# Kernel optimization log

Hardware: AMD Instinct MI355X
Metric: run time of the kernel (lower is better)

## Reference

```python
import jax, jax.numpy as jnp
import numpy as np

TT_SHAPES = [16, 16, 16, 16, 16, 16]
TT_RANKS = [1, 64, 64, 64, 64, 64, 1]
OUT_FEATURES = 4096  # 16*16*16
IN_FEATURES = 4096   # 16*16*16
N_TOKENS = 8192


def setup_inputs() -> dict:
    key = jax.random.key(0)
    ks = jax.random.split(key, len(TT_SHAPES) + 2)
    inp = {}
    for i in range(len(TT_SHAPES)):
        shape = (TT_RANKS[i], TT_SHAPES[i], TT_RANKS[i + 1])
        # xavier-uniform-like init
        fan = TT_RANKS[i] * TT_SHAPES[i] + TT_SHAPES[i] * TT_RANKS[i + 1]
        bound = float(np.sqrt(6.0 / fan))
        inp[f"core{i}"] = jax.random.uniform(ks[i], shape, jnp.float32, -bound, bound)
    inp["x"] = jax.random.normal(ks[-2], (N_TOKENS, IN_FEATURES), dtype=jnp.float32)
    b_bound = 1.0 / np.sqrt(IN_FEATURES)
    inp["b"] = jax.random.uniform(ks[-1], (OUT_FEATURES,), jnp.float32, -b_bound, b_bound)
    return inp


def _recover_weight(cores):
    # chain of reshape+matmul contractions, exactly as TTLinearR._recover_weight
    w = cores[0]
    for i in range(1, len(cores)):
        w = w.reshape(-1, TT_RANKS[i]) @ cores[i].reshape(TT_RANKS[i], -1)
    return w.reshape(OUT_FEATURES, IN_FEATURES)


def reference(x, core0, core1, core2, core3, core4, core5, b):
    w = _recover_weight([core0, core1, core2, core3, core4, core5])
    # F.linear(x, w, b) == x @ w.T + b
    return x @ w.T + b
```

## Files before the change

kernel.cpp:

```cpp
#include <hip/hip_runtime.h>


#define TOK 8192
#define DIN 4096
#define DOUT 4096
#define RNK 64

#define TB 16
#define BK 256
#define NKI (DIN / BK)
#define XS 264
#define TSTR 66

#define G2M 128
#define G2N 256
#define AS 72

typedef __bf16 bf16x8 __attribute__((ext_vector_type(8)));
typedef float f32x4 __attribute__((ext_vector_type(4)));
typedef float f32x16 __attribute__((ext_vector_type(16)));

__device__ __forceinline__ unsigned short f2bf(float f) {
  unsigned int u = __float_as_uint(f);
  u += 0x7FFFu + ((u >> 16) & 1u);
  return (unsigned short)(u >> 16);
}

__global__ void chain1(const float* __restrict__ c0, const float* __restrict__ c1,
                       const float* __restrict__ c4, const float* __restrict__ c5,
                       float* __restrict__ S1, float* __restrict__ S3) {
  int b = blockIdx.x;
  if (b < 64) {
    int idx = b * 256 + threadIdx.x;
    int m = idx >> 10, n = idx & 1023;
    const float* a = c0 + m * 64;
    float acc = 0.f;
#pragma unroll
    for (int k = 0; k < 64; ++k) acc += a[k] * c1[k * 1024 + n];
    S1[idx] = acc;
  } else {
    int idx = (b - 64) * 256 + threadIdx.x;
    int m = idx >> 4, n = idx & 15;
    const float* a = c4 + m * 64;
    float acc = 0.f;
#pragma unroll
    for (int k = 0; k < 64; ++k) acc += a[k] * c5[k * 16 + n];
    S3[idx] = acc;
  }
}

__global__ void chain2(const float* __restrict__ S1, const float* __restrict__ c2,
                       const float* __restrict__ c3, const float* __restrict__ S3,
                       unsigned short* __restrict__ Abf, unsigned short* __restrict__ Bbf) {
  int b = blockIdx.x;
  if (b < 1024) {
    int idx = b * 256 + threadIdx.x;
    int m = idx >> 10, n = idx & 1023;
    const float* a = S1 + m * 64;
    float acc = 0.f;
#pragma unroll
    for (int k = 0; k < 64; ++k) acc += a[k] * c2[k * 1024 + n];
    Abf[idx] = f2bf(acc);
  } else {
    int idx = (b - 1024) * 256 + threadIdx.x;
    int m = idx >> 8, n = idx & 255;
    const float* a = c3 + m * 64;
    float acc = 0.f;
#pragma unroll
    for (int k = 0; k < 64; ++k) acc += a[k] * S3[k * 256 + n];
    Bbf[idx] = f2bf(acc);
  }
}

__global__ __launch_bounds__(512)
void gemm1_t(const float* __restrict__ x, const unsigned short* __restrict__ Bbf,
             unsigned short* __restrict__ tb) {
  __shared__ __align__(16) unsigned short sm[(TB + 64) * XS];
  unsigned short* xs = sm;
  unsigned short* bs = sm + TB * XS;
  float* tred = (float*)sm;

  const int tid = threadIdx.x;
  const int m0 = blockIdx.x * TB;
  const int lane = tid & 63, wv = tid >> 6;
  const int r = lane & 15, q = lane >> 4;
  const int khalf = wv >> 2, jrank = wv & 3;

  int xr[2], xc[2], br[4], bc[4];
#pragma unroll
  for (int j = 0; j < 2; ++j) {
    int f = j * 512 + tid;
    xr[j] = f >> 6; xc[j] = f & 63;
  }
#pragma unroll
  for (int j = 0; j < 4; ++j) {
    int f = j * 512 + tid;
    br[j] = f >> 5; bc[j] = f & 31;
  }

  float4 px[2]; uint4 pb[4];
#pragma unroll
  for (int j = 0; j < 2; ++j)
    px[j] = *(const float4*)&x[(size_t)(m0 + xr[j]) * DIN + xc[j] * 4];
#pragma unroll
  for (int j = 0; j < 4; ++j)
    pb[j] = *(const uint4*)&Bbf[(size_t)br[j] * DIN + bc[j] * 8];

  f32x4 acc1 = (f32x4){0.f, 0.f, 0.f, 0.f};

#pragma unroll 1
  for (int ki = 0; ki < NKI; ++ki) {
    __syncthreads();
#pragma unroll
    for (int j = 0; j < 2; ++j) {
      ushort4 h = {f2bf(px[j].x), f2bf(px[j].y), f2bf(px[j].z), f2bf(px[j].w)};
      *(ushort4*)&xs[xr[j] * XS + xc[j] * 4] = h;
    }
#pragma unroll
    for (int j = 0; j < 4; ++j)
      *(uint4*)&bs[br[j] * XS + bc[j] * 8] = pb[j];
    if (ki + 1 < NKI) {
      int k0n = (ki + 1) * BK;
#pragma unroll
      for (int j = 0; j < 2; ++j)
        px[j] = *(const float4*)&x[(size_t)(m0 + xr[j]) * DIN + k0n + xc[j] * 4];
#pragma unroll
      for (int j = 0; j < 4; ++j)
        pb[j] = *(const uint4*)&Bbf[(size_t)br[j] * DIN + k0n + bc[j] * 8];
    }
    __syncthreads();
#pragma unroll
    for (int s32 = 0; s32 < 4; ++s32) {
      const int koff = khalf * 128 + s32 * 32 + q * 8;
      bf16x8 afr = *(const bf16x8*)&xs[r * XS + koff];
      bf16x8 bfr = *(const bf16x8*)&bs[(jrank * 16 + r) * XS + koff];
      acc1 = __builtin_amdgcn_mfma_f32_16x16x32_bf16(afr, bfr, acc1, 0, 0, 0);
    }
  }

  __syncthreads();
  if (wv >= 4) {
#pragma unroll
    for (int g = 0; g < 4; ++g)
      tred[(q * 4 + g) * TSTR + jrank * 16 + r] = acc1[g];
  }
  __syncthreads();
  if (wv < 4) {
#pragma unroll
    for (int g = 0; g < 4; ++g) {
      float v = acc1[g] + tred[(q * 4 + g) * TSTR + jrank * 16 + r];
      tb[(size_t)(m0 + q * 4 + g) * RNK + jrank * 16 + r] = f2bf(v);
    }
  }
}

__global__ __launch_bounds__(512)
void gemm2_y(const unsigned short* __restrict__ tbf, const unsigned short* __restrict__ Abf,
             const float* __restrict__ bias, float* __restrict__ out) {
  __shared__ __align__(16) unsigned short sm[(G2M + G2N) * AS];
  unsigned short* ts = sm;
  unsigned short* as_ = sm + G2M * AS;

  const int tid = threadIdx.x;
  const int m0 = blockIdx.y * G2M, n0 = blockIdx.x * G2N;
  const int lane = tid & 63, wv = tid >> 6;
  const int l31 = lane & 31, hi = lane >> 5;
  const int mw = (wv >> 1) * 32, nw = (wv & 1) * 128;

#pragma unroll
  for (int j = 0; j < 2; ++j) {
    int f = j * 512 + tid;
    int row = f >> 3, c = f & 7;
    *(uint4*)&ts[row * AS + c * 8] = *(const uint4*)&tbf[(size_t)(m0 + row) * RNK + c * 8];
  }
#pragma unroll
  for (int j = 0; j < 4; ++j) {
    int f = j * 512 + tid;
    int row = f >> 3, c = f & 7;
    *(uint4*)&as_[row * AS + c * 8] = *(const uint4*)&Abf[(size_t)(n0 + row) * RNK + c * 8];
  }
  __syncthreads();

  f32x16 acc[4];
#pragma unroll
  for (int j = 0; j < 4; ++j)
#pragma unroll
    for (int e = 0; e < 16; ++e) acc[j][e] = 0.f;

#pragma unroll
  for (int ks = 0; ks < 4; ++ks) {
    bf16x8 a = *(const bf16x8*)&ts[(mw + l31) * AS + ks * 16 + hi * 8];
#pragma unroll
    for (int j = 0; j < 4; ++j) {
      bf16x8 b = *(const bf16x8*)&as_[(nw + j * 32 + l31) * AS + ks * 16 + hi * 8];
      acc[j] = __builtin_amdgcn_mfma_f32_32x32x16_bf16(a, b, acc[j], 0, 0, 0);
    }
  }

  float bb[4];
#pragma unroll
  for (int j = 0; j < 4; ++j) bb[j] = bias[n0 + nw + j * 32 + l31];

#pragma unroll
  for (int j = 0; j < 4; ++j) {
    const int col = n0 + nw + j * 32 + l31;
#pragma unroll
    for (int reg = 0; reg < 16; ++reg) {
      int rowt = (reg & 3) + 8 * (reg >> 2) + 4 * hi;
      out[(size_t)(m0 + mw + rowt) * DOUT + col] = acc[j][reg] + bb[j];
    }
  }
}

extern "C" void kernel_launch(void* const* d_in, const int* in_sizes, int n_in,
                              void* d_out, int out_size, void* d_ws, size_t ws_size,
                              hipStream_t stream) {
  const float* c0 = (const float*)d_in[0];
  const float* c1 = (const float*)d_in[1];
  const float* c2 = (const float*)d_in[2];
  const float* c3 = (const float*)d_in[3];
  const float* c4 = (const float*)d_in[4];
  const float* c5 = (const float*)d_in[5];
  const float* x  = (const float*)d_in[6];
  const float* bias = (const float*)d_in[7];
  float* out = (float*)d_out;

  char* ws = (char*)d_ws;
  float*          S1  = (float*)(ws);
  float*          S3  = (float*)(ws + (1u << 16));
  unsigned short* Abf = (unsigned short*)(ws + (2u << 16));
  unsigned short* Bbf = (unsigned short*)(ws + (2u << 16) + (1u << 19));
  unsigned short* tbf = (unsigned short*)(ws + (2u << 16) + (2u << 19));

  chain1<<<128, 256, 0, stream>>>(c0, c1, c4, c5, S1, S3);
  chain2<<<2048, 256, 0, stream>>>(S1, c2, c3, S3, Abf, Bbf);
  gemm1_t<<<TOK / TB, 512, 0, stream>>>(x, Bbf, tbf);
  gemm2_y<<<dim3(DOUT / G2N, TOK / G2M), 512, 0, stream>>>(tbf, Abf, bias, out);
}
```

Measured before the change: 324.9 us.

## Drop LDS staging in both low-rank GEMMs, load fragments directly from global

The first GEMM (x times Bbf) now splits K across the 8 waves. Each wave loads its x and Bbf MFMA fragments straight from global memory, and the partial sums are reduced through shared memory at the end. This removes the per-iteration LDS staging and barriers. The second GEMM drops its shared-memory tiles too: each wave keeps its tb fragments in registers and streams Abf fragments from global (L2) over a smaller 128-column tile. In exchange there is more uncoalesced global and L2 traffic, and a larger end-of-kernel reduction buffer that may limit occupancy.

After: 283.5 us. 12.7% less time.

```diff
diff --git a/kernel.cpp b/kernel.cpp
--- a/kernel.cpp
+++ b/kernel.cpp
@@ -5,16 +5,6 @@
 #define DIN 4096
 #define DOUT 4096
 #define RNK 64
-
-#define TB 16
-#define BK 256
-#define NKI (DIN / BK)
-#define XS 264
-#define TSTR 66
-
-#define G2M 128
-#define G2N 256
-#define AS 72
 
 typedef __bf16 bf16x8 __attribute__((ext_vector_type(8)));
 typedef float f32x4 __attribute__((ext_vector_type(4)));
@@ -72,142 +62,105 @@
   }
 }
 
-__global__ __launch_bounds__(512)
-void gemm1_t(const float* __restrict__ x, const unsigned short* __restrict__ Bbf,
+__global__ __launch_bounds__(512, 4)
+void gemm1_s(const float* __restrict__ x, const unsigned short* __restrict__ Bbf,
              unsigned short* __restrict__ tb) {
-  __shared__ __align__(16) unsigned short sm[(TB + 64) * XS];
-  unsigned short* xs = sm;
-  unsigned short* bs = sm + TB * XS;
-  float* tred = (float*)sm;
+  __shared__ float red[8 * 1024];
 
   const int tid = threadIdx.x;
-  const int m0 = blockIdx.x * TB;
+  const int m0 = blockIdx.x * 16;
   const int lane = tid & 63, wv = tid >> 6;
   const int r = lane & 15, q = lane >> 4;
-  const int khalf = wv >> 2, jrank = wv & 3;
+  const size_t xrow = (size_t)(m0 + r) * DIN;
+  const int k0w = wv * 512;
 
-  int xr[2], xc[2], br[4], bc[4];
+  f32x4 acc[4];
 #pragma unroll
-  for (int j = 0; j < 2; ++j) {
-    int f = j * 512 + tid;
-    xr[j] = f >> 6; xc[j] = f & 63;
-  }
+  for (int j = 0; j < 4; ++j) acc[j] = (f32x4){0.f, 0.f, 0.f, 0.f};
+
 #pragma unroll
-  for (int j = 0; j < 4; ++j) {
-    int f = j * 512 + tid;
-    br[j] = f >> 5; bc[j] = f & 31;
-  }
-
-  float4 px[2]; uint4 pb[4];
+  for (int st = 0; st < 16; ++st) {
+    const int k0 = k0w + st * 32 + q * 8;
+    float4 xa = *(const float4*)&x[xrow + k0];
+    float4 xb = *(const float4*)&x[xrow + k0 + 4];
+    bf16x8 a;
+    a[0] = (__bf16)xa.x; a[1] = (__bf16)xa.y; a[2] = (__bf16)xa.z; a[3] = (__bf16)xa.w;
+    a[4] = (__bf16)xb.x; a[5] = (__bf16)xb.y; a[6] = (__bf16)xb.z; a[7] = (__bf16)xb.w;
 #pragma unroll
-  for (int j = 0; j < 2; ++j)
-    px[j] = *(const float4*)&x[(size_t)(m0 + xr[j]) * DIN + xc[j] * 4];
-#pragma unroll
-  for (int j = 0; j < 4; ++j)
-    pb[j] = *(const uint4*)&Bbf[(size_t)br[j] * DIN + bc[j] * 8];
-
-  f32x4 acc1 = (f32x4){0.f, 0.f, 0.f, 0.f};
-
-#pragma unroll 1
-  for (int ki = 0; ki < NKI; ++ki) {
-    __syncthreads();
-#pragma unroll
-    for (int j = 0; j < 2; ++j) {
-      ushort4 h = {f2bf(px[j].x), f2bf(px[j].y), f2bf(px[j].z), f2bf(px[j].w)};
-      *(ushort4*)&xs[xr[j] * XS + xc[j] * 4] = h;
-    }
-#pragma unroll
-    for (int j = 0; j < 4; ++j)
-      *(uint4*)&bs[br[j] * XS + bc[j] * 8] = pb[j];
-    if (ki + 1 < NKI) {
-      int k0n = (ki + 1) * BK;
-#pragma unroll
-      for (int j = 0; j < 2; ++j)
-        px[j] = *(const float4*)&x[(size_t)(m0 + xr[j]) * DIN + k0n + xc[j] * 4];
-#pragma unroll
-      for (int j = 0; j < 4; ++j)
-        pb[j] = *(const uint4*)&Bbf[(size_t)br[j] * DIN + k0n + bc[j] * 8];
-    }
-    __syncthreads();
-#pragma unroll
-    for (int s32 = 0; s32 < 4; ++s32) {
-      const int koff = khalf * 128 + s32 * 32 + q * 8;
-      bf16x8 afr = *(const bf16x8*)&xs[r * XS + koff];
-      bf16x8 bfr = *(const bf16x8*)&bs[(jrank * 16 + r) * XS + koff];
-      acc1 = __builtin_amdgcn_mfma_f32_16x16x32_bf16(afr, bfr, acc1, 0, 0, 0);
+    for (int j = 0; j < 4; ++j) {
+      bf16x8 b = *(const bf16x8*)&Bbf[(size_t)(j * 16 + r) * DIN + k0];
+      acc[j] = __builtin_amdgcn_mfma_f32_16x16x32_bf16(a, b, acc[j], 0, 0, 0);
     }
   }
 
-  __syncthreads();
-  if (wv >= 4) {
-#pragma unroll
-    for (int g = 0; g < 4; ++g)
-      tred[(q * 4 + g) * TSTR + jrank * 16 + r] = acc1[g];
-  }
-  __syncthreads();
-  if (wv < 4) {
-#pragma unroll
-    for (int g = 0; g < 4; ++g) {
-      float v = acc1[g] + tred[(q * 4 + g) * TSTR + jrank * 16 + r];
-      tb[(size_t)(m0 + q * 4 + g) * RNK + jrank * 16 + r] = f2bf(v);
-    }
-  }
-}
-
-__global__ __launch_bounds__(512)
-void gemm2_y(const unsigned short* __restrict__ tbf, const unsigned short* __restrict__ Abf,
-             const float* __restrict__ bias, float* __restrict__ out) {
-  __shared__ __align__(16) unsigned short sm[(G2M + G2N) * AS];
-  unsigned short* ts = sm;
-  unsigned short* as_ = sm + G2M * AS;
-
-  const int tid = threadIdx.x;
-  const int m0 = blockIdx.y * G2M, n0 = blockIdx.x * G2N;
-  const int lane = tid & 63, wv = tid >> 6;
-  const int l31 = lane & 31, hi = lane >> 5;
-  const int mw = (wv >> 1) * 32, nw = (wv & 1) * 128;
-
-#pragma unroll
-  for (int j = 0; j < 2; ++j) {
-    int f = j * 512 + tid;
-    int row = f >> 3, c = f & 7;
-    *(uint4*)&ts[row * AS + c * 8] = *(const uint4*)&tbf[(size_t)(m0 + row) * RNK + c * 8];
-  }
-#pragma unroll
-  for (int j = 0; j < 4; ++j) {
-    int f = j * 512 + tid;
-    int row = f >> 3, c = f & 7;
-    *(uint4*)&as_[row * AS + c * 8] = *(const uint4*)&Abf[(size_t)(n0 + row) * RNK + c * 8];
-  }
-  __syncthreads();
-
-  f32x16 acc[4];
+  float* myred = red + wv * 1024;
 #pragma unroll
   for (int j = 0; j < 4; ++j)
 #pragma unroll
-    for (int e = 0; e < 16; ++e) acc[j][e] = 0.f;
+    for (int g = 0; g < 4; ++g)
+      myred[(q * 4 + g) * 64 + j * 16 + r] = acc[j][g];
+  __syncthreads();
 
+  const int o = tid * 2;
+  float s0 = 0.f, s1 = 0.f;
 #pragma unroll
-  for (int ks = 0; ks < 4; ++ks) {
-    bf16x8 a = *(const bf16x8*)&ts[(mw + l31) * AS + ks * 16 + hi * 8];
-#pragma unroll
-    for (int j = 0; j < 4; ++j) {
-      bf16x8 b = *(const bf16x8*)&as_[(nw + j * 32 + l31) * AS + ks * 16 + hi * 8];
-      acc[j] = __builtin_amdgcn_mfma_f32_32x32x16_bf16(a, b, acc[j], 0, 0, 0);
-    }
+  for (int w = 0; w < 8; ++w) {
+    s0 += red[w * 1024 + o];
+    s1 += red[w * 1024 + o + 1];
   }
+  ushort2 h = {f2bf(s0), f2bf(s1)};
+  *(ushort2*)&tb[(size_t)m0 * RNK + o] = h;
+}
+
+__global__ __launch_bounds__(256, 4)
+void gemm2_s(const unsigned short* __restrict__ tb, const unsigned short* __restrict__ Abf,
+             const float* __restrict__ bias, float* __restrict__ out) {
+  const int tid = threadIdx.x;
+  const int lane = tid & 63, wv = tid >> 6;
+  const int l31 = lane & 31, hi = lane >> 5;
+  const int n0 = blockIdx.x * 128;
+  const int mb = blockIdx.y * 256;
 
   float bb[4];
 #pragma unroll
-  for (int j = 0; j < 4; ++j) bb[j] = bias[n0 + nw + j * 32 + l31];
+  for (int n = 0; n < 4; ++n) bb[n] = bias[n0 + n * 32 + l31];
+
+#pragma unroll 1
+  for (int s = 0; s < 2; ++s) {
+    const int m0 = mb + s * 128 + wv * 32;
+    bf16x8 ta[4];
+#pragma unroll
+    for (int ks = 0; ks < 4; ++ks)
+      ta[ks] = *(const bf16x8*)&tb[(size_t)(m0 + l31) * RNK + ks * 16 + hi * 8];
+
+#pragma unroll 1
+    for (int np = 0; np < 2; ++np) {
+      f32x16 acc[2];
+#pragma unroll
+      for (int j = 0; j < 2; ++j)
+#pragma unroll
+        for (int e = 0; e < 16; ++e) acc[j][e] = 0.f;
 
 #pragma unroll
-  for (int j = 0; j < 4; ++j) {
-    const int col = n0 + nw + j * 32 + l31;
+      for (int ks = 0; ks < 4; ++ks) {
 #pragma unroll
-    for (int reg = 0; reg < 16; ++reg) {
-      int rowt = (reg & 3) + 8 * (reg >> 2) + 4 * hi;
-      out[(size_t)(m0 + mw + rowt) * DOUT + col] = acc[j][reg] + bb[j];
+        for (int j = 0; j < 2; ++j) {
+          const int nrow = n0 + (np * 2 + j) * 32 + l31;
+          bf16x8 b = *(const bf16x8*)&Abf[(size_t)nrow * RNK + ks * 16 + hi * 8];
+          acc[j] = __builtin_amdgcn_mfma_f32_32x32x16_bf16(ta[ks], b, acc[j], 0, 0, 0);
+        }
+      }
+
+#pragma unroll
+      for (int j = 0; j < 2; ++j) {
+        const int col = n0 + (np * 2 + j) * 32 + l31;
+        const float bj = bb[np * 2 + j];
+#pragma unroll
+        for (int reg = 0; reg < 16; ++reg) {
+          const int rowt = (reg & 3) + 8 * (reg >> 2) + 4 * hi;
+          out[(size_t)(m0 + rowt) * DOUT + col] = acc[j][reg] + bj;
+        }
+      }
     }
   }
 }
@@ -234,6 +187,6 @@
 
   chain1<<<128, 256, 0, stream>>>(c0, c1, c4, c5, S1, S3);
   chain2<<<2048, 256, 0, stream>>>(S1, c2, c3, S3, Abf, Bbf);
-  gemm1_t<<<TOK / TB, 512, 0, stream>>>(x, Bbf, tbf);
-  gemm2_y<<<dim3(DOUT / G2N, TOK / G2M), 512, 0, stream>>>(tbf, Abf, bias, out);
+  gemm1_s<<<TOK / 16, 512, 0, stream>>>(x, Bbf, tbf);
+  gemm2_s<<<dim3(DOUT / 128, TOK / 256), 256, 0, stream>>>(tbf, Abf, bias, out);
 }
```
